# Performance work log

Hardware: AMD Instinct MI355X
Metric: run time of the kernel (lower is better)

## Reference

```python
import jax, jax.numpy as jnp
import numpy as np

# Multi-scale feature pyramid (H, W) per level: strides 8/16/32/64 on a ~512px image
SHAPES = ((64, 64), (32, 32), (16, 16), (8, 8))
N_HEADS, N_LEVELS, N_POINTS = 8, 4, 4
D_MODEL = 256
HEAD_DIM = D_MODEL // N_HEADS


def setup_inputs() -> dict:
    key = jax.random.key(0)
    ks = jax.random.split(key, 11)
    B, C = 4, D_MODEL
    Lv = sum(h * w for h, w in SHAPES)  # 5440
    Lq = Lv  # encoder self-attention: queries are the flattened features
    scale = 0.02
    return {
        "query": jax.random.normal(ks[0], (B, Lq, C), jnp.float32),
        "reference_points": jax.random.uniform(ks[1], (B, Lq, N_LEVELS, 2), jnp.float32),
        "value": jax.random.normal(ks[2], (B, Lv, C), jnp.float32),
        "W_off": jax.random.normal(ks[3], (C, N_HEADS * N_LEVELS * N_POINTS * 2), jnp.float32) * scale,
        "b_off": jax.random.normal(ks[4], (N_HEADS * N_LEVELS * N_POINTS * 2,), jnp.float32) * 0.5,
        "W_attn": jax.random.normal(ks[5], (C, N_HEADS * N_LEVELS * N_POINTS), jnp.float32) * scale,
        "b_attn": jax.random.normal(ks[6], (N_HEADS * N_LEVELS * N_POINTS,), jnp.float32) * scale,
        "W_val": jax.random.normal(ks[7], (C, C), jnp.float32) * scale,
        "b_val": jax.random.normal(ks[8], (C,), jnp.float32) * scale,
        "W_out": jax.random.normal(ks[9], (C, C), jnp.float32) * scale,
        "b_out": jax.random.normal(ks[10], (C,), jnp.float32) * scale,
    }


def _bilinear_sample(val, grid, H, W):
    """Replicates F.grid_sample(mode='bilinear', padding_mode='zeros', align_corners=False).

    val:  [N, C, H, W]
    grid: [N, Lq, P, 2] in [-1, 1] (x, y order)
    returns: [N, C, Lq, P]
    """
    N, C = val.shape[0], val.shape[1]
    # unnormalize (align_corners=False)
    x = (grid[..., 0] + 1.0) * 0.5 * W - 0.5  # [N, Lq, P]
    y = (grid[..., 1] + 1.0) * 0.5 * H - 0.5
    x0 = jnp.floor(x)
    y0 = jnp.floor(y)
    wx = x - x0  # fractional parts
    wy = y - y0
    flat = val.reshape(N, C, H * W)

    def gather(xi, yi):
        valid = (xi >= 0) & (xi < W) & (yi >= 0) & (yi < H)
        xc = jnp.clip(xi, 0, W - 1).astype(jnp.int32)
        yc = jnp.clip(yi, 0, H - 1).astype(jnp.int32)
        idx = yc * W + xc  # [N, Lq, P]
        g = jax.vmap(lambda v, i: v[:, i])(flat, idx)  # [N, C, Lq, P]
        return g * valid[:, None, :, :].astype(val.dtype)

    out = (gather(x0, y0) * ((1 - wx) * (1 - wy))[:, None]
           + gather(x0 + 1, y0) * (wx * (1 - wy))[:, None]
           + gather(x0, y0 + 1) * ((1 - wx) * wy)[:, None]
           + gather(x0 + 1, y0 + 1) * (wx * wy)[:, None])
    return out


def _ms_deform_attn(query, reference_points, value, W_off, b_off, W_attn, b_attn,
                    W_val, b_val, W_out, b_out):
    B, Lq, C = query.shape
    val = value @ W_val + b_val  # [B, Lv, C]
    val = val.reshape(B, -1, N_HEADS, HEAD_DIM)

    offsets = (query @ W_off + b_off).reshape(B, Lq, N_HEADS, N_LEVELS, N_POINTS, 2)
    weights = jax.nn.softmax(
        (query @ W_attn + b_attn).reshape(B, Lq, N_HEADS, N_LEVELS * N_POINTS), axis=-1
    ).reshape(B, Lq, N_HEADS, N_LEVELS, N_POINTS)

    # offset normalizer: (W, H) per level
    offset_norm = jnp.array([[w, h] for h, w in SHAPES], jnp.float32)
    # ref_dim == 2 branch
    locs = reference_points[:, :, None, :, None, :] + offsets / offset_norm[None, None, None, :, None, :]
    grids = 2.0 * locs - 1.0  # [B, Lq, nh, nl, np, 2]

    acc = jnp.zeros((B * N_HEADS, HEAD_DIM, Lq), query.dtype)
    start = 0
    for lid, (H, W) in enumerate(SHAPES):
        # [B, HW, nh, hd] -> [B*nh, hd, H, W]
        v = val[:, start:start + H * W].transpose(0, 2, 3, 1).reshape(B * N_HEADS, HEAD_DIM, H, W)
        g = grids[:, :, :, lid].transpose(0, 2, 1, 3, 4).reshape(B * N_HEADS, Lq, N_POINTS, 2)
        s = _bilinear_sample(v, g, H, W)  # [B*nh, hd, Lq, np]
        w = weights[:, :, :, lid].transpose(0, 2, 1, 3).reshape(B * N_HEADS, 1, Lq, N_POINTS)
        acc = acc + (s * w).sum(-1)
        start += H * W

    out = acc.reshape(B, D_MODEL, Lq).transpose(0, 2, 1)  # [B, Lq, C]
    return out @ W_out + b_out


def reference(query, reference_points, value, W_off, b_off, W_attn, b_attn,
              W_val, b_val, W_out, b_out):
    return _ms_deform_attn(query, reference_points, value, W_off, b_off,
                           W_attn, b_attn, W_val, b_val, W_out, b_out)
```

## Files before the change

### kernel.cpp

```cpp
#include <hip/hip_runtime.h>


typedef __attribute__((ext_vector_type(8))) _Float16 half8;
typedef __attribute__((ext_vector_type(4))) float f32x4;

typedef __attribute__((address_space(3))) unsigned int lds_uint;
typedef const __attribute__((address_space(1))) unsigned int g_uint;

__device__ __forceinline__ void load_lds16(const _Float16* g, _Float16* l) {
    __builtin_amdgcn_global_load_lds((g_uint*)g, (lds_uint*)l, 16, 0, 0);
}

__device__ __forceinline__ half8 splat8(_Float16 v) {
    half8 r = {v, v, v, v, v, v, v, v};
    return r;
}

#define M_TOTAL 21760

__global__ __launch_bounds__(256) void prep_cvt(
    const float* __restrict__ W_val, const float* __restrict__ W_off,
    const float* __restrict__ W_attn, const float* __restrict__ W_out,
    const float* __restrict__ b_off, const float* __restrict__ b_attn,
    const float* __restrict__ value, const float* __restrict__ query,
    _Float16* __restrict__ wt_val, _Float16* __restrict__ wt_qcat,
    _Float16* __restrict__ wt_out, float* __restrict__ bcat,
    _Float16* __restrict__ val16, _Float16* __restrict__ q16)
{
    const int r = blockIdx.x;
    const int k = threadIdx.x;
    if (r < 897) {
        if (r < 256) {
            wt_val[r * 256 + k] = (_Float16)W_val[k * 256 + r];
        } else if (r < 640) {
            const int n = r - 256;
            const float v = (n < 256) ? W_off[k * 256 + n] : W_attn[k * 128 + (n - 256)];
            wt_qcat[n * 256 + k] = (_Float16)v;
        } else if (r < 896) {
            const int n = r - 640;
            wt_out[n * 256 + k] = (_Float16)W_out[k * 256 + n];
        } else {
            bcat[k] = b_off[k];
            if (k < 128) bcat[256 + k] = b_attn[k];
        }
        return;
    }
    const size_t per = (size_t)M_TOTAL * 256 / 8;
    size_t idx = (size_t)(r - 897) * 256 + k;
    const float* src;
    _Float16* dst;
    if (idx < per) { src = value; dst = val16; }
    else { src = query; dst = q16; idx -= per; }
    const float4 lo = *(const float4*)(src + idx * 8);
    const float4 hi = *(const float4*)(src + idx * 8 + 4);
    half8 o = {(_Float16)lo.x, (_Float16)lo.y, (_Float16)lo.z, (_Float16)lo.w,
               (_Float16)hi.x, (_Float16)hi.y, (_Float16)hi.z, (_Float16)hi.w};
    *(half8*)(dst + idx * 8) = o;
}

__device__ __forceinline__ void gemm_core(
    const _Float16* __restrict__ A, const _Float16* __restrict__ Bt,
    const float* __restrict__ bias, void* __restrict__ Cv,
    int NN, int outf16, int mt, int nt)
{
    __shared__ _Float16 Ah[128 * 32];
    __shared__ _Float16 Bh[64 * 32];

    const int tid = threadIdx.x;
    const int bm = mt * 128;
    const int bn = nt * 64;
    const int wave = tid >> 6, lane = tid & 63;
    const int wm = (wave & 1) * 64, wn = (wave >> 1) * 32;
    const int ml = lane & 15, kq = (lane >> 4) * 8;
    const int lr = lane >> 2;
    const int lk = (lane & 3) * 8;

    const f32x4 zero4 = {0.f, 0.f, 0.f, 0.f};
    f32x4 acc[4][2];
#pragma unroll
    for (int i = 0; i < 4; ++i)
#pragma unroll
        for (int j = 0; j < 2; ++j) acc[i][j] = zero4;

    for (int kt = 0; kt < 8; ++kt) {
        const int k0 = kt * 32;
        __syncthreads();
#pragma unroll
        for (int t = 0; t < 2; ++t) {
            const int row = wave * 32 + t * 16;
            load_lds16(A + (size_t)(bm + row + lr) * 256 + k0 + lk,
                       Ah + (size_t)row * 32);
        }
        {
            const int row = wave * 16;
            load_lds16(Bt + (size_t)(bn + row + lr) * 256 + k0 + lk,
                       Bh + (size_t)row * 32);
        }
        __syncthreads();

        half8 af[4], bf[2];
#pragma unroll
        for (int i = 0; i < 4; ++i)
            af[i] = *(const half8*)(Ah + (wm + i * 16 + ml) * 32 + kq);
#pragma unroll
        for (int j = 0; j < 2; ++j)
            bf[j] = *(const half8*)(Bh + (wn + j * 16 + ml) * 32 + kq);
#pragma unroll
        for (int i = 0; i < 4; ++i)
#pragma unroll
            for (int j = 0; j < 2; ++j)
                acc[i][j] = __builtin_amdgcn_mfma_f32_16x16x32_f16(af[i], bf[j], acc[i][j], 0, 0, 0);
    }

    const int r0 = (lane >> 4) * 4;
#pragma unroll
    for (int j = 0; j < 2; ++j) {
        const int col = bn + wn + j * 16 + ml;
        const float bj = bias[col];
#pragma unroll
        for (int i = 0; i < 4; ++i) {
            const size_t rbase = (size_t)(bm + wm + i * 16 + r0) * NN + col;
#pragma unroll
            for (int r = 0; r < 4; ++r) {
                const float v = acc[i][j][r] + bj;
                if (outf16)
                    ((_Float16*)Cv)[rbase + (size_t)r * NN] = (_Float16)v;
                else
                    ((float*)Cv)[rbase + (size_t)r * NN] = v;
            }
        }
    }
}

__global__ __launch_bounds__(256) void gemm12(
    const _Float16* __restrict__ val16, const _Float16* __restrict__ q16,
    const _Float16* __restrict__ wtv, const _Float16* __restrict__ wtq,
    const float* __restrict__ b_val, const float* __restrict__ bcat,
    _Float16* __restrict__ valh, _Float16* __restrict__ offh)
{
    int id = blockIdx.x;
    if (id < 680) {
        gemm_core(val16, wtv, b_val, valh, 256, 1, id >> 2, id & 3);
    } else {
        id -= 680;
        gemm_core(q16, wtq, bcat, offh, 384, 1, id / 6, id % 6);
    }
}

__global__ __launch_bounds__(256) void gemm_single(
    const _Float16* __restrict__ A, const _Float16* __restrict__ Bt,
    const float* __restrict__ bias, void* __restrict__ Cv, int NN, int outf16)
{
    const int id = blockIdx.x;
    gemm_core(A, Bt, bias, Cv, NN, outf16, id >> 2, id & 3);
}

__global__ __launch_bounds__(256) void sample_f16(
    const _Float16* __restrict__ valh,
    const float* __restrict__ refp,
    const _Float16* __restrict__ offh,
    _Float16* __restrict__ acc_out)
{
    const int wave = threadIdx.x >> 6, lane = threadIdx.x & 63;
    const int q2 = lane >> 5, sl = lane & 31;
    const int bq = blockIdx.x * 8 + wave * 2 + q2;
    const int b = bq / 5440;
    const int h = sl >> 2;
    const int d8 = (sl & 3) * 8;

    const _Float16* off_row = offh + (size_t)bq * 384 + h * 32;
    const _Float16* att_row = offh + (size_t)bq * 384 + 256 + h * 16;
    const float* rp = refp + (size_t)bq * 8;

    float offv[32];
#pragma unroll
    for (int i = 0; i < 4; ++i) {
        const half8 t = *(const half8*)(off_row + i * 8);
#pragma unroll
        for (int j = 0; j < 8; ++j) offv[i * 8 + j] = (float)t[j];
    }
    float lg[16];
    {
        const half8 t0 = *(const half8*)(att_row);
        const half8 t1 = *(const half8*)(att_row + 8);
#pragma unroll
        for (int j = 0; j < 8; ++j) { lg[j] = (float)t0[j]; lg[8 + j] = (float)t1[j]; }
    }
    float mx = -1e30f;
#pragma unroll
    for (int i = 0; i < 16; ++i) mx = fmaxf(mx, lg[i]);
    float s = 0.f;
#pragma unroll
    for (int i = 0; i < 16; ++i) { lg[i] = __expf(lg[i] - mx); s += lg[i]; }
    const float inv = 1.f / s;

    const float4 rp01 = *(const float4*)rp;
    const float4 rp23 = *(const float4*)(rp + 4);
    const float rxs[4] = {rp01.x, rp01.z, rp23.x, rp23.z};
    const float rys[4] = {rp01.y, rp01.w, rp23.y, rp23.w};

    const int Ws_[4] = {64, 32, 16, 8};
    const int starts_[4] = {0, 4096, 5120, 5376};

    half8 acc = splat8((_Float16)0.f);
#pragma unroll
    for (int l = 0; l < 4; ++l) {
        const int W = Ws_[l];
        const float fW = (float)W;
        const _Float16* vbase = valh + ((size_t)(b * 5440 + starts_[l])) * 256 + h * 32 + d8;
        const float rx = rxs[l], ry = rys[l];
#pragma unroll
        for (int p = 0; p < 4; ++p) {
            const int pi = l * 4 + p;
            const float aw = lg[pi] * inv;
            const float x = fmaf(rx, fW, offv[pi * 2 + 0]) - 0.5f;
            const float y = fmaf(ry, fW, offv[pi * 2 + 1]) - 0.5f;
            const float x0f = floorf(x), y0f = floorf(y);
            const int x0 = (int)x0f, y0 = (int)y0f;
            const float wx = x - x0f, wy = y - y0f;
            const bool okx0 = ((unsigned)x0 < (unsigned)W);
            const bool okx1 = ((unsigned)(x0 + 1) < (unsigned)W);
            const bool oky0 = ((unsigned)y0 < (unsigned)W);
            const bool oky1 = ((unsigned)(y0 + 1) < (unsigned)W);
            const int xc0 = min(max(x0, 0), W - 1);
            const int xc1 = min(max(x0 + 1, 0), W - 1);
            const int yc0 = min(max(y0, 0), W - 1);
            const int yc1 = min(max(y0 + 1, 0), W - 1);
            const float w00 = (okx0 & oky0) ? (1.f - wx) * (1.f - wy) * aw : 0.f;
            const float w10 = (okx1 & oky0) ? wx * (1.f - wy) * aw : 0.f;
            const float w01 = (okx0 & oky1) ? (1.f - wx) * wy * aw : 0.f;
            const float w11 = (okx1 & oky1) ? wx * wy * aw : 0.f;

            const half8 c00 = *(const half8*)(vbase + (size_t)(yc0 * W + xc0) * 256);
            const half8 c10 = *(const half8*)(vbase + (size_t)(yc0 * W + xc1) * 256);
            const half8 c01 = *(const half8*)(vbase + (size_t)(yc1 * W + xc0) * 256);
            const half8 c11 = *(const half8*)(vbase + (size_t)(yc1 * W + xc1) * 256);

            acc += c00 * splat8((_Float16)w00);
            acc += c10 * splat8((_Float16)w10);
            acc += c01 * splat8((_Float16)w01);
            acc += c11 * splat8((_Float16)w11);
        }
    }

    *(half8*)(acc_out + (size_t)bq * 256 + h * 32 + d8) = acc;
}

extern "C" void kernel_launch(void* const* d_in, const int* in_sizes, int n_in,
                              void* d_out, int out_size, void* d_ws, size_t ws_size,
                              hipStream_t stream) {
    const float* query  = (const float*)d_in[0];
    const float* refp   = (const float*)d_in[1];
    const float* value  = (const float*)d_in[2];
    const float* W_off  = (const float*)d_in[3];
    const float* b_off  = (const float*)d_in[4];
    const float* W_attn = (const float*)d_in[5];
    const float* b_attn = (const float*)d_in[6];
    const float* W_val  = (const float*)d_in[7];
    const float* b_val  = (const float*)d_in[8];
    const float* W_out  = (const float*)d_in[9];
    const float* b_out  = (const float*)d_in[10];
    float* out = (float*)d_out;

    const size_t M = M_TOTAL;

    _Float16* val16 = (_Float16*)d_ws;
    _Float16* q16   = val16 + M * 256;
    _Float16* valh  = q16 + M * 256;
    _Float16* offh  = valh + M * 256;
    _Float16* wtv   = offh + M * 384;
    _Float16* wtq   = wtv + 256 * 256;
    _Float16* wto   = wtq + 384 * 256;
    float* bcat     = (float*)(wto + 256 * 256);
    _Float16* acc16 = val16;

    dim3 blk(256);
    prep_cvt<<<dim3(897 + 5440), blk, 0, stream>>>(
        W_val, W_off, W_attn, W_out, b_off, b_attn, value, query,
        wtv, wtq, wto, bcat, val16, q16);
    gemm12<<<dim3(1700), blk, 0, stream>>>(val16, q16, wtv, wtq, b_val, bcat, valh, offh);
    sample_f16<<<dim3(M / 8), blk, 0, stream>>>(valh, refp, offh, acc16);
    gemm_single<<<dim3(680), blk, 0, stream>>>(acc16, wto, b_out, out, 256, 0);
}
```

Baseline: 186.2 us.

## Fuse deformable sampling with output projection via LDS-staged MFMA

Merges the sampling kernel and the final output GEMM into one kernel. Each block samples 16 queries into a shared-memory tile, then runs MFMA 16x16x32 against the W_out weights and writes fp32 output with bias. This drops one launch and the fp16 round trip of the accumulated features through global memory. The trade-offs are fewer blocks (M/16), each block re-reading the full W_out from global or L2, and a block-wide sync between sampling and the matmul.

```diff
diff --git a/kernel.cpp b/kernel.cpp
--- a/kernel.cpp
+++ b/kernel.cpp
@@ -143,107 +143,132 @@
         gemm_core(val16, wtv, b_val, valh, 256, 1, id >> 2, id & 3);
     } else {
         id -= 680;
-        gemm_core(q16, wtq, bcat, offh, 384, 1, id / 6, id % 6);
-    }
-}
-
-__global__ __launch_bounds__(256) void gemm_single(
-    const _Float16* __restrict__ A, const _Float16* __restrict__ Bt,
-    const float* __restrict__ bias, void* __restrict__ Cv, int NN, int outf16)
-{
-    const int id = blockIdx.x;
-    gemm_core(A, Bt, bias, Cv, NN, outf16, id >> 2, id & 3);
-}
-
-__global__ __launch_bounds__(256) void sample_f16(
+        gemm_core(q16, wtq, bcat, offh, 384, 1, (id - 0) / 6, (id - 0) % 6);
+    }
+}
+
+__global__ __launch_bounds__(256) void sample_out(
     const _Float16* __restrict__ valh,
     const float* __restrict__ refp,
     const _Float16* __restrict__ offh,
-    _Float16* __restrict__ acc_out)
+    const _Float16* __restrict__ wto,
+    const float* __restrict__ b_out,
+    float* __restrict__ out)
 {
+    __shared__ _Float16 accL[16 * 264];
+
+    const int q0 = blockIdx.x * 16;
     const int wave = threadIdx.x >> 6, lane = threadIdx.x & 63;
     const int q2 = lane >> 5, sl = lane & 31;
-    const int bq = blockIdx.x * 8 + wave * 2 + q2;
-    const int b = bq / 5440;
     const int h = sl >> 2;
     const int d8 = (sl & 3) * 8;
 
-    const _Float16* off_row = offh + (size_t)bq * 384 + h * 32;
-    const _Float16* att_row = offh + (size_t)bq * 384 + 256 + h * 16;
-    const float* rp = refp + (size_t)bq * 8;
-
-    float offv[32];
-#pragma unroll
-    for (int i = 0; i < 4; ++i) {
-        const half8 t = *(const half8*)(off_row + i * 8);
-#pragma unroll
-        for (int j = 0; j < 8; ++j) offv[i * 8 + j] = (float)t[j];
-    }
-    float lg[16];
-    {
-        const half8 t0 = *(const half8*)(att_row);
-        const half8 t1 = *(const half8*)(att_row + 8);
-#pragma unroll
-        for (int j = 0; j < 8; ++j) { lg[j] = (float)t0[j]; lg[8 + j] = (float)t1[j]; }
-    }
-    float mx = -1e30f;
-#pragma unroll
-    for (int i = 0; i < 16; ++i) mx = fmaxf(mx, lg[i]);
-    float s = 0.f;
-#pragma unroll
-    for (int i = 0; i < 16; ++i) { lg[i] = __expf(lg[i] - mx); s += lg[i]; }
-    const float inv = 1.f / s;
-
-    const float4 rp01 = *(const float4*)rp;
-    const float4 rp23 = *(const float4*)(rp + 4);
-    const float rxs[4] = {rp01.x, rp01.z, rp23.x, rp23.z};
-    const float rys[4] = {rp01.y, rp01.w, rp23.y, rp23.w};
-
     const int Ws_[4] = {64, 32, 16, 8};
     const int starts_[4] = {0, 4096, 5120, 5376};
 
-    half8 acc = splat8((_Float16)0.f);
-#pragma unroll
-    for (int l = 0; l < 4; ++l) {
-        const int W = Ws_[l];
-        const float fW = (float)W;
-        const _Float16* vbase = valh + ((size_t)(b * 5440 + starts_[l])) * 256 + h * 32 + d8;
-        const float rx = rxs[l], ry = rys[l];
-#pragma unroll
-        for (int p = 0; p < 4; ++p) {
-            const int pi = l * 4 + p;
-            const float aw = lg[pi] * inv;
-            const float x = fmaf(rx, fW, offv[pi * 2 + 0]) - 0.5f;
-            const float y = fmaf(ry, fW, offv[pi * 2 + 1]) - 0.5f;
-            const float x0f = floorf(x), y0f = floorf(y);
-            const int x0 = (int)x0f, y0 = (int)y0f;
-            const float wx = x - x0f, wy = y - y0f;
-            const bool okx0 = ((unsigned)x0 < (unsigned)W);
-            const bool okx1 = ((unsigned)(x0 + 1) < (unsigned)W);
-            const bool oky0 = ((unsigned)y0 < (unsigned)W);
-            const bool oky1 = ((unsigned)(y0 + 1) < (unsigned)W);
-            const int xc0 = min(max(x0, 0), W - 1);
-            const int xc1 = min(max(x0 + 1, 0), W - 1);
-            const int yc0 = min(max(y0, 0), W - 1);
-            const int yc1 = min(max(y0 + 1, 0), W - 1);
-            const float w00 = (okx0 & oky0) ? (1.f - wx) * (1.f - wy) * aw : 0.f;
-            const float w10 = (okx1 & oky0) ? wx * (1.f - wy) * aw : 0.f;
-            const float w01 = (okx0 & oky1) ? (1.f - wx) * wy * aw : 0.f;
-            const float w11 = (okx1 & oky1) ? wx * wy * aw : 0.f;
-
-            const half8 c00 = *(const half8*)(vbase + (size_t)(yc0 * W + xc0) * 256);
-            const half8 c10 = *(const half8*)(vbase + (size_t)(yc0 * W + xc1) * 256);
-            const half8 c01 = *(const half8*)(vbase + (size_t)(yc1 * W + xc0) * 256);
-            const half8 c11 = *(const half8*)(vbase + (size_t)(yc1 * W + xc1) * 256);
-
-            acc += c00 * splat8((_Float16)w00);
-            acc += c10 * splat8((_Float16)w10);
-            acc += c01 * splat8((_Float16)w01);
-            acc += c11 * splat8((_Float16)w11);
-        }
-    }
-
-    *(half8*)(acc_out + (size_t)bq * 256 + h * 32 + d8) = acc;
+    for (int pass = 0; pass < 2; ++pass) {
+        const int ql = pass * 8 + wave * 2 + q2;
+        const int bq = q0 + ql;
+        const int b = bq / 5440;
+
+        const _Float16* off_row = offh + (size_t)bq * 384 + h * 32;
+        const _Float16* att_row = offh + (size_t)bq * 384 + 256 + h * 16;
+        const float* rp = refp + (size_t)bq * 8;
+
+        float offv[32];
+#pragma unroll
+        for (int i = 0; i < 4; ++i) {
+            const half8 t = *(const half8*)(off_row + i * 8);
+#pragma unroll
+            for (int j = 0; j < 8; ++j) offv[i * 8 + j] = (float)t[j];
+        }
+        float lg[16];
+        {
+            const half8 t0 = *(const half8*)(att_row);
+            const half8 t1 = *(const half8*)(att_row + 8);
+#pragma unroll
+            for (int j = 0; j < 8; ++j) { lg[j] = (float)t0[j]; lg[8 + j] = (float)t1[j]; }
+        }
+        float mx = -1e30f;
+#pragma unroll
+        for (int i = 0; i < 16; ++i) mx = fmaxf(mx, lg[i]);
+        float s = 0.f;
+#pragma unroll
+        for (int i = 0; i < 16; ++i) { lg[i] = __expf(lg[i] - mx); s += lg[i]; }
+        const float inv = 1.f / s;
+
+        const float4 rp01 = *(const float4*)rp;
+        const float4 rp23 = *(const float4*)(rp + 4);
+        const float rxs[4] = {rp01.x, rp01.z, rp23.x, rp23.z};
+        const float rys[4] = {rp01.y, rp01.w, rp23.y, rp23.w};
+
+        half8 acc = splat8((_Float16)0.f);
+#pragma unroll
+        for (int l = 0; l < 4; ++l) {
+            const int W = Ws_[l];
+            const float fW = (float)W;
+            const _Float16* vbase = valh + ((size_t)(b * 5440 + starts_[l])) * 256 + h * 32 + d8;
+            const float rx = rxs[l], ry = rys[l];
+#pragma unroll
+            for (int p = 0; p < 4; ++p) {
+                const int pi = l * 4 + p;
+                const float aw = lg[pi] * inv;
+                const float x = fmaf(rx, fW, offv[pi * 2 + 0]) - 0.5f;
+                const float y = fmaf(ry, fW, offv[pi * 2 + 1]) - 0.5f;
+                const float x0f = floorf(x), y0f = floorf(y);
+                const int x0 = (int)x0f, y0 = (int)y0f;
+                const float wx = x - x0f, wy = y - y0f;
+                const bool okx0 = ((unsigned)x0 < (unsigned)W);
+                const bool okx1 = ((unsigned)(x0 + 1) < (unsigned)W);
+                const bool oky0 = ((unsigned)y0 < (unsigned)W);
+                const bool oky1 = ((unsigned)(y0 + 1) < (unsigned)W);
+                const int xc0 = min(max(x0, 0), W - 1);
+                const int xc1 = min(max(x0 + 1, 0), W - 1);
+                const int yc0 = min(max(y0, 0), W - 1);
+                const int yc1 = min(max(y0 + 1, 0), W - 1);
+                const float w00 = (okx0 & oky0) ? (1.f - wx) * (1.f - wy) * aw : 0.f;
+                const float w10 = (okx1 & oky0) ? wx * (1.f - wy) * aw : 0.f;
+                const float w01 = (okx0 & oky1) ? (1.f - wx) * wy * aw : 0.f;
+                const float w11 = (okx1 & oky1) ? wx * wy * aw : 0.f;
+
+                const half8 c00 = *(const half8*)(vbase + (size_t)(yc0 * W + xc0) * 256);
+                const half8 c10 = *(const half8*)(vbase + (size_t)(yc0 * W + xc1) * 256);
+                const half8 c01 = *(const half8*)(vbase + (size_t)(yc1 * W + xc0) * 256);
+                const half8 c11 = *(const half8*)(vbase + (size_t)(yc1 * W + xc1) * 256);
+
+                acc += c00 * splat8((_Float16)w00);
+                acc += c10 * splat8((_Float16)w10);
+                acc += c01 * splat8((_Float16)w01);
+                acc += c11 * splat8((_Float16)w11);
+            }
+        }
+
+        *(half8*)(accL + ql * 264 + h * 32 + d8) = acc;
+    }
+
+    __syncthreads();
+
+    const int ml = lane & 15, kq = (lane >> 4) * 8;
+    const f32x4 zero4 = {0.f, 0.f, 0.f, 0.f};
+    f32x4 acc3[4] = {zero4, zero4, zero4, zero4};
+#pragma unroll
+    for (int kt = 0; kt < 8; ++kt) {
+        const half8 af = *(const half8*)(accL + ml * 264 + kt * 32 + kq);
+#pragma unroll
+        for (int j = 0; j < 4; ++j) {
+            const half8 bf = *(const half8*)(wto + (size_t)(wave * 64 + j * 16 + ml) * 256 + kt * 32 + kq);
+            acc3[j] = __builtin_amdgcn_mfma_f32_16x16x32_f16(af, bf, acc3[j], 0, 0, 0);
+        }
+    }
+    const int r0 = (lane >> 4) * 4;
+#pragma unroll
+    for (int j = 0; j < 4; ++j) {
+        const int col = wave * 64 + j * 16 + ml;
+        const float bj = b_out[col];
+#pragma unroll
+        for (int r = 0; r < 4; ++r)
+            out[(size_t)(q0 + r0 + r) * 256 + col] = acc3[j][r] + bj;
+    }
 }
 
 extern "C" void kernel_launch(void* const* d_in, const int* in_sizes, int n_in,
@@ -272,13 +297,11 @@
     _Float16* wtq   = wtv + 256 * 256;
     _Float16* wto   = wtq + 384 * 256;
     float* bcat     = (float*)(wto + 256 * 256);
-    _Float16* acc16 = val16;
 
     dim3 blk(256);
     prep_cvt<<<dim3(897 + 5440), blk, 0, stream>>>(
         W_val, W_off, W_attn, W_out, b_off, b_attn, value, query,
         wtv, wtq, wto, bcat, val16, q16);
     gemm12<<<dim3(1700), blk, 0, stream>>>(val16, q16, wtv, wtq, b_val, bcat, valh, offh);
-    sample_f16<<<dim3(M / 8), blk, 0, stream>>>(valh, refp, offh, acc16);
-    gemm_single<<<dim3(680), blk, 0, stream>>>(acc16, wto, b_out, out, 256, 0);
-}
+    sample_out<<<dim3(M / 16), blk, 0, stream>>>(valh, refp, offh, wto, b_out, out);
+}
```

Result: slower. 199.1 us (+6.9%).

## Fuse fp32-to-fp16 conversion into projection GEMM and drop prep kernel

Applied to the files above, without the earlier changes.

Removes the separate prep kernel that converted value, query and weights to fp16. The first GEMM now loads fp32 activations and weights directly, converts them in registers and stores them to padded LDS tiles. The W_out transpose/convert moves into the sampling kernel. This saves one launch and a full fp16 write+read round trip of both activation tensors, at the cost of twice the global load bytes for A, strided uncoalesced-ish weight loads, and losing the async global_load_lds path.

```diff
diff --git a/kernel.cpp b/kernel.cpp
--- a/kernel.cpp
+++ b/kernel.cpp
@@ -18,50 +18,106 @@
 
 #define M_TOTAL 21760
 
-__global__ __launch_bounds__(256) void prep_cvt(
+__global__ __launch_bounds__(256) void gemm12_cvt(
+    const float* __restrict__ value, const float* __restrict__ query,
     const float* __restrict__ W_val, const float* __restrict__ W_off,
-    const float* __restrict__ W_attn, const float* __restrict__ W_out,
-    const float* __restrict__ b_off, const float* __restrict__ b_attn,
-    const float* __restrict__ value, const float* __restrict__ query,
-    _Float16* __restrict__ wt_val, _Float16* __restrict__ wt_qcat,
-    _Float16* __restrict__ wt_out, float* __restrict__ bcat,
-    _Float16* __restrict__ val16, _Float16* __restrict__ q16)
+    const float* __restrict__ W_attn,
+    const float* __restrict__ b_val, const float* __restrict__ b_off,
+    const float* __restrict__ b_attn,
+    _Float16* __restrict__ valh, _Float16* __restrict__ offh)
 {
-    const int r = blockIdx.x;
-    const int k = threadIdx.x;
-    if (r < 897) {
-        if (r < 256) {
-            wt_val[r * 256 + k] = (_Float16)W_val[k * 256 + r];
-        } else if (r < 640) {
-            const int n = r - 256;
-            const float v = (n < 256) ? W_off[k * 256 + n] : W_attn[k * 128 + (n - 256)];
-            wt_qcat[n * 256 + k] = (_Float16)v;
-        } else if (r < 896) {
-            const int n = r - 640;
-            wt_out[n * 256 + k] = (_Float16)W_out[k * 256 + n];
-        } else {
-            bcat[k] = b_off[k];
-            if (k < 128) bcat[256 + k] = b_attn[k];
-        }
-        return;
-    }
-    const size_t per = (size_t)M_TOTAL * 256 / 8;
-    size_t idx = (size_t)(r - 897) * 256 + k;
-    const float* src;
-    _Float16* dst;
-    if (idx < per) { src = value; dst = val16; }
-    else { src = query; dst = q16; idx -= per; }
-    const float4 lo = *(const float4*)(src + idx * 8);
-    const float4 hi = *(const float4*)(src + idx * 8 + 4);
-    half8 o = {(_Float16)lo.x, (_Float16)lo.y, (_Float16)lo.z, (_Float16)lo.w,
-               (_Float16)hi.x, (_Float16)hi.y, (_Float16)hi.z, (_Float16)hi.w};
-    *(half8*)(dst + idx * 8) = o;
+    __shared__ _Float16 As[128 * 34];
+    __shared__ _Float16 Bs[64 * 34];
+
+    const bool g1 = blockIdx.x < 680;
+    const int id = g1 ? blockIdx.x : blockIdx.x - 680;
+    const int mt = g1 ? (id >> 2) : (id / 6);
+    const int nt = g1 ? (id & 3) : (id % 6);
+    const int NN = g1 ? 256 : 384;
+    const float* A = g1 ? value : query;
+    _Float16* C = g1 ? valh : offh;
+    const int bm = mt * 128;
+    const int bn = nt * 64;
+
+    const float* W;
+    int sW, nb;
+    if (g1)           { W = W_val;  sW = 256; nb = bn; }
+    else if (bn < 256){ W = W_off;  sW = 256; nb = bn; }
+    else              { W = W_attn; sW = 128; nb = bn - 256; }
+
+    const int tid = threadIdx.x;
+    const int wave = tid >> 6, lane = tid & 63;
+    const int wm = (wave & 1) * 64, wn = (wave >> 1) * 32;
+    const int ml = lane & 15, kq = (lane >> 4) * 8;
+
+    const int ar = tid >> 1, akb = (tid & 1) * 16;
+    const int bn_l = tid & 63, bk8 = (tid >> 6) * 8;
+
+    const f32x4 zero4 = {0.f, 0.f, 0.f, 0.f};
+    f32x4 acc[4][2];
+#pragma unroll
+    for (int i = 0; i < 4; ++i)
+#pragma unroll
+        for (int j = 0; j < 2; ++j) acc[i][j] = zero4;
+
+    for (int kt = 0; kt < 8; ++kt) {
+        const int k0 = kt * 32;
+        const float* as = A + (size_t)(bm + ar) * 256 + k0 + akb;
+        const float4 a0 = *(const float4*)(as + 0);
+        const float4 a1 = *(const float4*)(as + 4);
+        const float4 a2 = *(const float4*)(as + 8);
+        const float4 a3 = *(const float4*)(as + 12);
+        float bv[8];
+#pragma unroll
+        for (int j = 0; j < 8; ++j)
+            bv[j] = W[(size_t)(k0 + bk8 + j) * sW + nb + bn_l];
+
+        const half8 ha0 = {(_Float16)a0.x, (_Float16)a0.y, (_Float16)a0.z, (_Float16)a0.w,
+                           (_Float16)a1.x, (_Float16)a1.y, (_Float16)a1.z, (_Float16)a1.w};
+        const half8 ha1 = {(_Float16)a2.x, (_Float16)a2.y, (_Float16)a2.z, (_Float16)a2.w,
+                           (_Float16)a3.x, (_Float16)a3.y, (_Float16)a3.z, (_Float16)a3.w};
+        const half8 hb = {(_Float16)bv[0], (_Float16)bv[1], (_Float16)bv[2], (_Float16)bv[3],
+                          (_Float16)bv[4], (_Float16)bv[5], (_Float16)bv[6], (_Float16)bv[7]};
+
+        __syncthreads();
+        *(half8*)(As + ar * 34 + akb) = ha0;
+        *(half8*)(As + ar * 34 + akb + 8) = ha1;
+        *(half8*)(Bs + bn_l * 34 + bk8) = hb;
+        __syncthreads();
+
+        half8 af[4], bf[2];
+#pragma unroll
+        for (int i = 0; i < 4; ++i)
+            af[i] = *(const half8*)(As + (wm + i * 16 + ml) * 34 + kq);
+#pragma unroll
+        for (int j = 0; j < 2; ++j)
+            bf[j] = *(const half8*)(Bs + (wn + j * 16 + ml) * 34 + kq);
+#pragma unroll
+        for (int i = 0; i < 4; ++i)
+#pragma unroll
+            for (int j = 0; j < 2; ++j)
+                acc[i][j] = __builtin_amdgcn_mfma_f32_16x16x32_f16(af[i], bf[j], acc[i][j], 0, 0, 0);
+    }
+
+    const int r0 = (lane >> 4) * 4;
+#pragma unroll
+    for (int j = 0; j < 2; ++j) {
+        const int col = bn + wn + j * 16 + ml;
+        const float bj = g1 ? b_val[col] : (col < 256 ? b_off[col] : b_attn[col - 256]);
+#pragma unroll
+        for (int i = 0; i < 4; ++i) {
+            const size_t rbase = (size_t)(bm + wm + i * 16 + r0) * NN + col;
+#pragma unroll
+            for (int r = 0; r < 4; ++r)
+                C[rbase + (size_t)r * NN] = (_Float16)(acc[i][j][r] + bj);
+        }
+    }
 }
 
 __device__ __forceinline__ void gemm_core(
     const _Float16* __restrict__ A, const _Float16* __restrict__ Bt,
-    const float* __restrict__ bias, void* __restrict__ Cv,
-    int NN, int outf16, int mt, int nt)
+    const float* __restrict__ bias, float* __restrict__ Cv,
+    int NN, int mt, int nt)
 {
     __shared__ _Float16 Ah[128 * 32];
     __shared__ _Float16 Bh[64 * 32];
@@ -121,46 +177,32 @@
         for (int i = 0; i < 4; ++i) {
             const size_t rbase = (size_t)(bm + wm + i * 16 + r0) * NN + col;
 #pragma unroll
-            for (int r = 0; r < 4; ++r) {
-                const float v = acc[i][j][r] + bj;
-                if (outf16)
-                    ((_Float16*)Cv)[rbase + (size_t)r * NN] = (_Float16)v;
-                else
-                    ((float*)Cv)[rbase + (size_t)r * NN] = v;
-            }
-        }
-    }
-}
-
-__global__ __launch_bounds__(256) void gemm12(
-    const _Float16* __restrict__ val16, const _Float16* __restrict__ q16,
-    const _Float16* __restrict__ wtv, const _Float16* __restrict__ wtq,
-    const float* __restrict__ b_val, const float* __restrict__ bcat,
-    _Float16* __restrict__ valh, _Float16* __restrict__ offh)
-{
-    int id = blockIdx.x;
-    if (id < 680) {
-        gemm_core(val16, wtv, b_val, valh, 256, 1, id >> 2, id & 3);
-    } else {
-        id -= 680;
-        gemm_core(q16, wtq, bcat, offh, 384, 1, id / 6, id % 6);
+            for (int r = 0; r < 4; ++r)
+                Cv[rbase + (size_t)r * NN] = acc[i][j][r] + bj;
+        }
     }
 }
 
 __global__ __launch_bounds__(256) void gemm_single(
     const _Float16* __restrict__ A, const _Float16* __restrict__ Bt,
-    const float* __restrict__ bias, void* __restrict__ Cv, int NN, int outf16)
+    const float* __restrict__ bias, float* __restrict__ Cv)
 {
     const int id = blockIdx.x;
-    gemm_core(A, Bt, bias, Cv, NN, outf16, id >> 2, id & 3);
+    gemm_core(A, Bt, bias, Cv, 256, id >> 2, id & 3);
 }
 
 __global__ __launch_bounds__(256) void sample_f16(
     const _Float16* __restrict__ valh,
     const float* __restrict__ refp,
     const _Float16* __restrict__ offh,
+    const float* __restrict__ W_out,
+    _Float16* __restrict__ wto,
     _Float16* __restrict__ acc_out)
 {
+    if (blockIdx.x < 256)
+        wto[blockIdx.x * 256 + threadIdx.x] =
+            (_Float16)W_out[threadIdx.x * 256 + blockIdx.x];
+
     const int wave = threadIdx.x >> 6, lane = threadIdx.x & 63;
     const int q2 = lane >> 5, sl = lane & 31;
     const int bq = blockIdx.x * 8 + wave * 2 + q2;
@@ -264,21 +306,14 @@
 
     const size_t M = M_TOTAL;
 
-    _Float16* val16 = (_Float16*)d_ws;
-    _Float16* q16   = val16 + M * 256;
-    _Float16* valh  = q16 + M * 256;
+    _Float16* valh  = (_Float16*)d_ws;
     _Float16* offh  = valh + M * 256;
-    _Float16* wtv   = offh + M * 384;
-    _Float16* wtq   = wtv + 256 * 256;
-    _Float16* wto   = wtq + 384 * 256;
-    float* bcat     = (float*)(wto + 256 * 256);
-    _Float16* acc16 = val16;
+    _Float16* acc16 = offh + M * 384;
+    _Float16* wto   = acc16 + M * 256;
 
     dim3 blk(256);
-    prep_cvt<<<dim3(897 + 5440), blk, 0, stream>>>(
-        W_val, W_off, W_attn, W_out, b_off, b_attn, value, query,
-        wtv, wtq, wto, bcat, val16, q16);
-    gemm12<<<dim3(1700), blk, 0, stream>>>(val16, q16, wtv, wtq, b_val, bcat, valh, offh);
-    sample_f16<<<dim3(M / 8), blk, 0, stream>>>(valh, refp, offh, acc16);
-    gemm_single<<<dim3(680), blk, 0, stream>>>(acc16, wto, b_out, out, 256, 0);
-}
+    gemm12_cvt<<<dim3(1700), blk, 0, stream>>>(
+        value, query, W_val, W_off, W_attn, b_val, b_off, b_attn, valh, offh);
+    sample_f16<<<dim3(M / 8), blk, 0, stream>>>(valh, refp, offh, W_out, wto, acc16);
+    gemm_single<<<dim3(680), blk, 0, stream>>>(acc16, wto, b_out, out);
+}
```

Measured after the change: 187.7 us. About the same (+0.8%).
